# Performance work log

Measured on AMD Instinct MI355X. Metric: run time of the kernel, lower is better.

The kernel has to match this reference:

```python
import jax, jax.numpy as jnp
import numpy as np

N = 100000   # nodes
E = 1000000  # edges
G = 64       # graphs in batch
DIN, DH, DOUT = 128, 128, 64
BN_EPS = 1e-5


def setup_inputs() -> dict:
    key = jax.random.key(0)
    ks = jax.random.split(key, 20)
    inp = {}
    inp['x'] = jax.random.normal(ks[0], (N, DIN), dtype=jnp.float32)
    inp['edge_index'] = jax.random.randint(ks[1], (2, E), 0, N, dtype=jnp.int64)
    inp['batch'] = jnp.sort(jax.random.randint(ks[2], (N,), 0, G, dtype=jnp.int64))
    # GCN conv weights (stored [in, out]) + biases
    s = lambda k, i, o: jax.random.normal(k, (i, o), dtype=jnp.float32) / np.sqrt(i)
    inp['W1'] = s(ks[3], DIN, DH);  inp['b1'] = jnp.zeros((DH,), jnp.float32)
    inp['W2'] = s(ks[4], DH, DH);   inp['b2'] = jnp.zeros((DH,), jnp.float32)
    inp['W3'] = s(ks[5], DH, DOUT); inp['b3'] = jnp.zeros((DOUT,), jnp.float32)
    # BatchNorm params/buffers (eval mode)
    inp['g1'] = jnp.ones((DH,), jnp.float32);  inp['beta1'] = jnp.zeros((DH,), jnp.float32)
    inp['g2'] = jnp.ones((DH,), jnp.float32);  inp['beta2'] = jnp.zeros((DH,), jnp.float32)
    inp['mean1'] = jnp.zeros((DH,), jnp.float32); inp['var1'] = jnp.ones((DH,), jnp.float32)
    inp['mean2'] = jnp.zeros((DH,), jnp.float32); inp['var2'] = jnp.ones((DH,), jnp.float32)
    # GlobalAttention gate_nn: Linear(DOUT,DH) ReLU Linear(DH,1)
    inp['Wg1'] = s(ks[6], DOUT, DH); inp['bg1'] = jnp.zeros((DH,), jnp.float32)
    inp['Wg2'] = s(ks[7], DH, 1);    inp['bg2'] = jnp.zeros((1,), jnp.float32)
    # head MLP: Linear(DOUT,DH) ReLU Linear(DH,DOUT)
    inp['Wm1'] = s(ks[8], DOUT, DH); inp['bm1'] = jnp.zeros((DH,), jnp.float32)
    inp['Wm2'] = s(ks[9], DH, DOUT); inp['bm2'] = jnp.zeros((DOUT,), jnp.float32)
    return inp


def _gcn_conv(x, W, b, src, dst):
    # PyG GCNConv: add self-loops, sym-normalize, linear, scatter-sum, bias
    h = x @ W                                            # [N, out]
    deg = jnp.ones((N,), h.dtype).at[dst].add(1.0)       # in-degree + self-loop
    dinv = jax.lax.rsqrt(deg)
    norm = dinv[src] * dinv[dst]                         # [E]
    msg = h[src] * norm[:, None]                         # gather + scale
    out = jax.ops.segment_sum(msg, dst, num_segments=N)  # scatter
    out = out + h * (dinv * dinv)[:, None]               # self-loop term
    return out + b


def _bn(x, g, beta, mean, var):
    return (x - mean) * jax.lax.rsqrt(var + BN_EPS) * g + beta


def reference(x, edge_index, batch, W1, b1, W2, b2, W3, b3,
              g1, beta1, g2, beta2, mean1, var1, mean2, var2,
              Wg1, bg1, Wg2, bg2, Wm1, bm1, Wm2, bm2):
    src, dst = edge_index[0], edge_index[1]
    h = jax.nn.relu(_bn(_gcn_conv(x, W1, b1, src, dst), g1, beta1, mean1, var1))
    h = jax.nn.relu(_bn(_gcn_conv(h, W2, b2, src, dst), g2, beta2, mean2, var2))
    h = _gcn_conv(h, W3, b3, src, dst)                   # [N, DOUT]
    # GlobalAttention pooling: per-graph softmax of gate scores
    gate = jax.nn.relu(h @ Wg1 + bg1) @ Wg2 + bg2        # [N, 1]
    gate = gate[:, 0]
    m = jax.ops.segment_max(gate, batch, num_segments=G)
    e = jnp.exp(gate - m[batch])
    s = jax.ops.segment_sum(e, batch, num_segments=G)
    a = e / s[batch]                                     # [N]
    pooled = jax.ops.segment_sum(h * a[:, None], batch, num_segments=G)  # [G, DOUT]
    # MLP head (dropout off in eval)
    return jax.nn.relu(pooled @ Wm1 + bm1) @ Wm2 + bm2   # [G, DOUT]
```

## Files before the change

kernel.cpp:

```cpp
#include <hip/hip_runtime.h>
#include <hip/hip_bf16.h>
#include <hip/hip_fp16.h>
#include <math.h>

#define NN 100000
#define EE 1000000
#define GG 64
#define BN_EPS 1e-5f
#define CPB 16
#define EB 4096
#define NBLK ((EE + EB - 1) / EB)
#define NBUCK ((NN + 511) / 512)

typedef __attribute__((ext_vector_type(8))) short bf16x8;
typedef __attribute__((ext_vector_type(4))) float f32x4;

__device__ inline short f2bf(float f) {
  unsigned u = __float_as_uint(f);
  u = u + 0x7fff + ((u >> 16) & 1);
  return (short)(u >> 16);
}
__device__ inline float bf2f(short h) {
  return __uint_as_float(((unsigned)(unsigned short)h) << 16);
}

__device__ inline unsigned fenc(float f) {
  int b = __float_as_int(f);
  return (b < 0) ? ~(unsigned)b : ((unsigned)b | 0x80000000u);
}
__device__ inline float fdec(unsigned u) {
  int b = (u & 0x80000000u) ? (int)(u & 0x7fffffffu) : (int)~u;
  return __int_as_float(b);
}

__device__ inline void acc2(float& a0, float& a1, unsigned u) {
  asm("v_fma_mix_f32 %0, %2, 1.0, %0 op_sel:[0,0,0] op_sel_hi:[1,0,0]\n\t"
      "v_fma_mix_f32 %1, %2, 1.0, %1 op_sel:[1,0,0] op_sel_hi:[1,0,0]"
      : "+v"(a0), "+v"(a1)
      : "v"(u));
}
__device__ inline void acc8(float* a, uint4 u) {
  acc2(a[0], a[1], u.x);
  acc2(a[2], a[3], u.y);
  acc2(a[4], a[5], u.z);
  acc2(a[6], a[7], u.w);
}

__global__ __launch_bounds__(256) void k_bhist(const int* __restrict__ dst,
                                               int* __restrict__ bhist, int E) {
  __shared__ int h[256];
  int t = threadIdx.x;
  h[t] = 0;
  __syncthreads();
  int base = blockIdx.x * EB;
#pragma unroll
  for (int j = 0; j < EB / 256; ++j) {
    int i = base + j * 256 + t;
    if (i < E) atomicAdd(&h[dst[i] >> 9], 1);
  }
  __syncthreads();
  bhist[blockIdx.x * 256 + t] = h[t];
}

__global__ __launch_bounds__(256) void k_bscan1(int* __restrict__ bhist,
                                                int* __restrict__ btot) {
  __shared__ int s[256];
  int bin = blockIdx.x, t = threadIdx.x;
  int v = (t < NBLK) ? bhist[t * 256 + bin] : 0;
  s[t] = v;
  __syncthreads();
  for (int o = 1; o < 256; o <<= 1) {
    int u = (t >= o) ? s[t - o] : 0;
    __syncthreads();
    s[t] += u;
    __syncthreads();
  }
  if (t < NBLK) bhist[t * 256 + bin] = s[t] - v;
  if (t == 255) btot[bin] = s[255];
}

__global__ __launch_bounds__(256) void k_bscan2(const int* __restrict__ btot,
                                                int* __restrict__ bstart) {
  __shared__ int s[256];
  int t = threadIdx.x;
  int v = btot[t];
  s[t] = v;
  __syncthreads();
  for (int o = 1; o < 256; o <<= 1) {
    int u = (t >= o) ? s[t - o] : 0;
    __syncthreads();
    s[t] += u;
    __syncthreads();
  }
  bstart[t] = s[t] - v;
}

__global__ __launch_bounds__(256) void k_bscat(const int* __restrict__ src,
                                               const int* __restrict__ dst,
                                               const int* __restrict__ bhist,
                                               const int* __restrict__ bstart,
                                               int2* __restrict__ pairs, int E) {
  __shared__ int h[256];
  __shared__ int base[256];
  int t = threadIdx.x;
  h[t] = 0;
  __syncthreads();
  int b0 = blockIdx.x * EB;
  int ds[EB / 256], rk[EB / 256];
#pragma unroll
  for (int j = 0; j < EB / 256; ++j) {
    int i = b0 + j * 256 + t;
    if (i < E) {
      int d = dst[i];
      ds[j] = d;
      rk[j] = atomicAdd(&h[d >> 9], 1);
    } else
      ds[j] = -1;
  }
  __syncthreads();
  base[t] = bstart[t] + bhist[blockIdx.x * 256 + t];
  __syncthreads();
#pragma unroll
  for (int j = 0; j < EB / 256; ++j) {
    int i = b0 + j * 256 + t;
    if (ds[j] >= 0) {
      int pos = base[ds[j] >> 9] + rk[j];
      pairs[pos] = make_int2(src[i], ds[j]);
    }
  }
}

__global__ __launch_bounds__(256) void k_bfill(const int2* __restrict__ pairs,
                                               const int* __restrict__ bstart,
                                               int* __restrict__ rowstart,
                                               int* __restrict__ eidx,
                                               float* __restrict__ dinv, int N,
                                               int E) {
  __shared__ int h[512];
  __shared__ int ex[512];
  __shared__ int ps[256];
  const int b = blockIdx.x;
  const int n0 = b << 9;
  const int e0 = bstart[b], e1 = bstart[b + 1];
  const int t = threadIdx.x;
  h[t] = 0;
  h[t + 256] = 0;
  __syncthreads();
  for (int i = e0 + t; i < e1; i += 256) atomicAdd(&h[pairs[i].y - n0], 1);
  __syncthreads();
  int v0 = h[2 * t], v1 = h[2 * t + 1];
  int sp = v0 + v1;
  ps[t] = sp;
  __syncthreads();
  for (int o = 1; o < 256; o <<= 1) {
    int u = (t >= o) ? ps[t - o] : 0;
    __syncthreads();
    ps[t] += u;
    __syncthreads();
  }
  int ex0 = ps[t] - sp;
  ex[2 * t] = ex0;
  ex[2 * t + 1] = ex0 + v0;
  __syncthreads();
  for (int i = t; i < 512; i += 256) {
    int node = n0 + i;
    if (node < N) {
      rowstart[node] = e0 + ex[i];
      dinv[node] = rsqrtf(1.0f + (float)h[i]);
    }
  }
  if (b == 0 && t == 0) rowstart[N] = E;
  __syncthreads();
  for (int i = e0 + t; i < e1; i += 256) {
    int2 p = pairs[i];
    int r = atomicAdd(&ex[p.y - n0], 1);
    eidx[e0 + r] = p.x;
  }
}

__global__ __launch_bounds__(256) void k_wsplit(const float* __restrict__ W1,
                                                const float* __restrict__ W2,
                                                const float* __restrict__ W3,
                                                const float* __restrict__ Wg1,
                                                short* __restrict__ wt) {
  int i = blockIdx.x * 256 + threadIdx.x;
  const float* W;
  short *hi, *lo;
  int K, M, idx;
  if (i < 16384) {
    W = W1; hi = wt; lo = wt + 16384; K = 128; M = 128; idx = i;
  } else if (i < 32768) {
    W = W2; hi = wt + 32768; lo = wt + 49152; K = 128; M = 128; idx = i - 16384;
  } else if (i < 40960) {
    W = W3; hi = wt + 65536; lo = wt + 73728; K = 128; M = 64; idx = i - 32768;
  } else {
    W = Wg1; hi = wt + 81920; lo = wt + 90112; K = 64; M = 128; idx = i - 40960;
  }
  int k = idx / M, n = idx % M;
  float w = W[idx];
  short h = f2bf(w);
  hi[n * K + k] = h;
  lo[n * K + k] = f2bf(w - bf2f(h));
}

__global__ __launch_bounds__(256) void k_bnprep(
    const float* __restrict__ g1, const float* __restrict__ b1,
    const float* __restrict__ m1, const float* __restrict__ v1,
    const float* __restrict__ g2, const float* __restrict__ b2,
    const float* __restrict__ m2, const float* __restrict__ v2,
    float* __restrict__ s1, float* __restrict__ h1, float* __restrict__ s2,
    float* __restrict__ h2) {
  int i = threadIdx.x;
  if (i < 128) {
    float s = g1[i] * rsqrtf(v1[i] + BN_EPS);
    s1[i] = s;
    h1[i] = b1[i] - m1[i] * s;
  } else {
    int j = i - 128;
    float s = g2[j] * rsqrtf(v2[j] + BN_EPS);
    s2[j] = s;
    h2[j] = b2[j] - m2[j] * s;
  }
}

template <int K, int M, int AIN, int DINV, int GATE, int OUTH>
__global__ __launch_bounds__(256, 2) void k_mgemm(
    const float* __restrict__ Xf, const short* __restrict__ Xhi,
    const short* __restrict__ Xlo, const short* __restrict__ Wthi,
    const short* __restrict__ Wtlo, const float* __restrict__ dinv,
    const float* __restrict__ gbias, const float* __restrict__ Wg2v,
    const float* __restrict__ bg2v, void* __restrict__ Y,
    float* __restrict__ gate, int nrows) {
  constexpr int NC = K / 32;
  constexpr int CT = M / 16;
  constexpr int R = 4;
  const int lane = threadIdx.x & 63;
  const int wave = threadIdx.x >> 6;
  const int m16 = lane & 15;
  const int quad = lane >> 4;
  const int rowbase = blockIdx.x * 256 + wave * 64;

  bf16x8 ahi[R][NC], alo[R][NC];
#pragma unroll
  for (int t = 0; t < R; ++t) {
    const int arow = rowbase + t * 16 + m16;
    const bool rok = arow < nrows;
#pragma unroll
    for (int c = 0; c < NC; ++c) {
      const int k0 = c * 32 + quad * 8;
      if constexpr (AIN) {
        if (rok) {
          ahi[t][c] = *(const bf16x8*)(Xhi + (size_t)arow * K + k0);
          alo[t][c] = *(const bf16x8*)(Xlo + (size_t)arow * K + k0);
        } else {
          ahi[t][c] = bf16x8{0, 0, 0, 0, 0, 0, 0, 0};
          alo[t][c] = bf16x8{0, 0, 0, 0, 0, 0, 0, 0};
        }
      } else {
        float4 v0 = make_float4(0.f, 0.f, 0.f, 0.f), v1 = v0;
        if (rok) {
          v0 = *(const float4*)(Xf + (size_t)arow * K + k0);
          v1 = *(const float4*)(Xf + (size_t)arow * K + k0 + 4);
        }
        float vv[8] = {v0.x, v0.y, v0.z, v0.w, v1.x, v1.y, v1.z, v1.w};
#pragma unroll
        for (int j = 0; j < 8; ++j) {
          short h = f2bf(vv[j]);
          ahi[t][c][j] = h;
          alo[t][c][j] = f2bf(vv[j] - bf2f(h));
        }
      }
    }
  }

  float dv[R][4];
  if constexpr (DINV && !GATE) {
#pragma unroll
    for (int t = 0; t < R; ++t)
#pragma unroll
      for (int r = 0; r < 4; ++r) {
        int row = rowbase + t * 16 + quad * 4 + r;
        dv[t][r] = (row < nrows) ? dinv[row] : 0.f;
      }
  }

  float gp[R][4];
  if constexpr (GATE) {
#pragma unroll
    for (int t = 0; t < R; ++t)
#pragma unroll
      for (int r = 0; r < 4; ++r) gp[t][r] = 0.f;
  }

#pragma unroll
  for (int ct = 0; ct < CT; ++ct) {
    bf16x8 bhi[NC], blo[NC];
    const size_t wrow = (size_t)(ct * 16 + m16) * K + quad * 8;
#pragma unroll
    for (int c = 0; c < NC; ++c) {
      bhi[c] = *(const bf16x8*)(Wthi + wrow + c * 32);
      blo[c] = *(const bf16x8*)(Wtlo + wrow + c * 32);
    }
#pragma unroll
    for (int t = 0; t < R; ++t) {
      f32x4 acc = {0.f, 0.f, 0.f, 0.f};
#pragma unroll
      for (int c = 0; c < NC; ++c) {
        acc = __builtin_amdgcn_mfma_f32_16x16x32_bf16(ahi[t][c], bhi[c], acc, 0, 0, 0);
        acc = __builtin_amdgcn_mfma_f32_16x16x32_bf16(ahi[t][c], blo[c], acc, 0, 0, 0);
        acc = __builtin_amdgcn_mfma_f32_16x16x32_bf16(alo[t][c], bhi[c], acc, 0, 0, 0);
      }
      if constexpr (GATE) {
        const int col = ct * 16 + m16;
        const float gb = gbias[col], wg = Wg2v[col];
#pragma unroll
        for (int r = 0; r < 4; ++r) gp[t][r] += fmaxf(acc[r] + gb, 0.f) * wg;
      } else {
#pragma unroll
        for (int r = 0; r < 4; ++r) {
          const int row = rowbase + t * 16 + quad * 4 + r;
          if (row < nrows) {
            float v = acc[r];
            if constexpr (DINV) v *= dv[t][r];
            if constexpr (OUTH)
              ((__half*)Y)[(size_t)row * M + ct * 16 + m16] = __float2half(v);
            else
              ((float*)Y)[(size_t)row * M + ct * 16 + m16] = v;
          }
        }
      }
    }
  }
  if constexpr (GATE) {
#pragma unroll
    for (int o = 1; o < 16; o <<= 1) {
#pragma unroll
      for (int t = 0; t < R; ++t)
#pragma unroll
        for (int r = 0; r < 4; ++r) gp[t][r] += __shfl_xor(gp[t][r], o, 64);
    }
    if (m16 == 0) {
      const float b2 = bg2v[0];
#pragma unroll
      for (int t = 0; t < R; ++t)
#pragma unroll
        for (int r = 0; r < 4; ++r) {
          const int row = rowbase + t * 16 + quad * 4 + r;
          if (row < nrows) gate[row] = gp[t][r] + b2;
        }
    }
  }
}

template <int M, int EPI>
__global__ __launch_bounds__(256) void k_agg(const __half* __restrict__ hp,
                                             const int* __restrict__ rowstart,
                                             const int* __restrict__ eidx,
                                             const float* __restrict__ dinv,
                                             const float* __restrict__ bias,
                                             const float* __restrict__ bns,
                                             const float* __restrict__ bnh,
                                             float* __restrict__ outf,
                                             short* __restrict__ ohi,
                                             short* __restrict__ olo, int N) {
  const int w = (blockIdx.x * 256 + threadIdx.x) >> 6;
  if (w >= N) return;
  const int lane = threadIdx.x & 63;
  constexpr int LPR = M / 8;
  constexpr int EPW = 64 / LPR;
  const int q = lane / LPR;
  const int sub = lane % LPR;
  const unsigned subo = (unsigned)sub * 16u;
  const float di = dinv[w];
  const int lo = rowstart[w], hi = rowstart[w + 1];
  const char* hpb = (const char*)hp;
  float a[8] = {0.f, 0.f, 0.f, 0.f, 0.f, 0.f, 0.f, 0.f};

  int e = lo + q;
  for (; e + EPW < hi; e += 2 * EPW) {
    int s0 = eidx[e], s1 = eidx[e + EPW];
    uint4 u0 = *(const uint4*)(hpb + ((unsigned)s0 * (unsigned)(M * 2) + subo));
    uint4 u1 = *(const uint4*)(hpb + ((unsigned)s1 * (unsigned)(M * 2) + subo));
    acc8(a, u0);
    acc8(a, u1);
  }
  for (; e < hi; e += EPW) {
    int s = eidx[e];
    uint4 u = *(const uint4*)(hpb + ((unsigned)s * (unsigned)(M * 2) + subo));
    acc8(a, u);
  }
#pragma unroll
  for (int o = LPR; o < 64; o <<= 1)
#pragma unroll
    for (int j = 0; j < 8; ++j) a[j] += __shfl_xor(a[j], o, 64);

  if (q != 0) return;
  uint4 us = *(const uint4*)(hpb + ((unsigned)w * (unsigned)(M * 2) + subo));
  acc8(a, us);
  float4 b0 = *(const float4*)(bias + sub * 8);
  float4 b1 = *(const float4*)(bias + sub * 8 + 4);
  float r[8];
  r[0] = a[0] * di + b0.x;
  r[1] = a[1] * di + b0.y;
  r[2] = a[2] * di + b0.z;
  r[3] = a[3] * di + b0.w;
  r[4] = a[4] * di + b1.x;
  r[5] = a[5] * di + b1.y;
  r[6] = a[6] * di + b1.z;
  r[7] = a[7] * di + b1.w;
  if constexpr (EPI) {
    float4 s0 = *(const float4*)(bns + sub * 8);
    float4 s1 = *(const float4*)(bns + sub * 8 + 4);
    float4 h0 = *(const float4*)(bnh + sub * 8);
    float4 h1 = *(const float4*)(bnh + sub * 8 + 4);
    float sv[8] = {s0.x, s0.y, s0.z, s0.w, s1.x, s1.y, s1.z, s1.w};
    float hv[8] = {h0.x, h0.y, h0.z, h0.w, h1.x, h1.y, h1.z, h1.w};
    short hs[8], ls[8];
#pragma unroll
    for (int j = 0; j < 8; ++j) {
      float ev = fmaxf(r[j] * sv[j] + hv[j], 0.f);
      short hb = f2bf(ev);
      float res = ev - bf2f(hb);
      hs[j] = hb;
      ls[j] = (short)(__float_as_uint(res) >> 16);
    }
    *(short4*)(ohi + (size_t)w * M + sub * 8) = make_short4(hs[0], hs[1], hs[2], hs[3]);
    *(short4*)(ohi + (size_t)w * M + sub * 8 + 4) = make_short4(hs[4], hs[5], hs[6], hs[7]);
    *(short4*)(olo + (size_t)w * M + sub * 8) = make_short4(ls[0], ls[1], ls[2], ls[3]);
    *(short4*)(olo + (size_t)w * M + sub * 8 + 4) = make_short4(ls[4], ls[5], ls[6], ls[7]);
  } else {
    *(float4*)(outf + (size_t)w * M + sub * 8) = make_float4(r[0], r[1], r[2], r[3]);
    *(float4*)(outf + (size_t)w * M + sub * 8 + 4) = make_float4(r[4], r[5], r[6], r[7]);
  }
}

__global__ __launch_bounds__(128) void k_gbounds(const int* __restrict__ batch,
                                                 int* __restrict__ gstart,
                                                 int N) {
  int g = threadIdx.x;
  if (g > GG) return;
  int lo = 0, hi = N;
  while (lo < hi) {
    int mid = (lo + hi) >> 1;
    if (batch[mid] < g) lo = mid + 1;
    else hi = mid;
  }
  gstart[g] = lo;
}

__global__ __launch_bounds__(256) void k_pmax(const float* __restrict__ gate,
                                              const int* __restrict__ gstart,
                                              unsigned* __restrict__ gmaxu) {
  __shared__ unsigned red[256];
  const int g = blockIdx.x / CPB;
  const int c = blockIdx.x % CPB;
  const int lo = gstart[g], hi = gstart[g + 1];
  const int len = hi - lo;
  const int b0 = lo + (int)(((long long)len * c) / CPB);
  const int b1 = lo + (int)(((long long)len * (c + 1)) / CPB);
  unsigned mx = 0u;
  for (int i = b0 + threadIdx.x; i < b1; i += 256) mx = max(mx, fenc(gate[i]));
  red[threadIdx.x] = mx;
  __syncthreads();
  for (int o = 128; o; o >>= 1) {
    if (threadIdx.x < o)
      red[threadIdx.x] = max(red[threadIdx.x], red[threadIdx.x + o]);
    __syncthreads();
  }
  if (threadIdx.x == 0 && red[0] != 0u) atomicMax(&gmaxu[g], red[0]);
}

__global__ __launch_bounds__(256) void k_psum(const float* __restrict__ gate,
                                              const float* __restrict__ h3,
                                              const unsigned* __restrict__ gmaxu,
                                              const int* __restrict__ gstart,
                                              float* __restrict__ pooledw,
                                              float* __restrict__ ssum) {
  __shared__ float accs[4][64];
  __shared__ float ses[4];
  const int g = blockIdx.x / CPB;
  const int c = blockIdx.x % CPB;
  const int lo = gstart[g], hi = gstart[g + 1];
  const int len = hi - lo;
  const int b0 = lo + (int)(((long long)len * c) / CPB);
  const int b1 = lo + (int)(((long long)len * (c + 1)) / CPB);
  const int wave = threadIdx.x >> 6, lane = threadIdx.x & 63;
  const float m = fdec(gmaxu[g]);
  float acc = 0.f, se = 0.f;
  for (int i = b0 + wave; i < b1; i += 4) {
    float e = expf(gate[i] - m);
    acc += e * h3[(size_t)i * 64 + lane];
    se += e;
  }
  accs[wave][lane] = acc;
  if (lane == 0) ses[wave] = se;
  __syncthreads();
  if (threadIdx.x < 64) {
    float a = accs[0][threadIdx.x] + accs[1][threadIdx.x] +
              accs[2][threadIdx.x] + accs[3][threadIdx.x];
    if (a != 0.f) atomicAdd(&pooledw[g * 64 + threadIdx.x], a);
  }
  if (threadIdx.x == 64) {
    float s = ses[0] + ses[1] + ses[2] + ses[3];
    if (s != 0.f) atomicAdd(&ssum[g], s);
  }
}

__global__ __launch_bounds__(256) void k_head(const float* __restrict__ pooledw,
                                              const float* __restrict__ ssum,
                                              const float* __restrict__ Wm1,
                                              const float* __restrict__ bm1,
                                              const float* __restrict__ Wm2,
                                              const float* __restrict__ bm2,
                                              float* __restrict__ out) {
  __shared__ float P[64 * 64];
  __shared__ float T[64 * 128];
  int tid = threadIdx.x;
  for (int i = tid; i < 4096; i += 256) {
    float s = ssum[i >> 6];
    P[i] = pooledw[i] * ((s > 0.f) ? 1.0f / s : 0.f);
  }
  __syncthreads();
  for (int e = tid; e < 8192; e += 256) {
    int r = e >> 7, c = e & 127;
    float a = bm1[c];
    for (int k = 0; k < 64; ++k) a += P[r * 64 + k] * Wm1[k * 128 + c];
    T[e] = fmaxf(a, 0.f);
  }
  __syncthreads();
  for (int e = tid; e < 4096; e += 256) {
    int r = e >> 6, c = e & 63;
    float a = bm2[c];
    for (int k = 0; k < 128; ++k) a += T[r * 128 + k] * Wm2[k * 64 + c];
    out[e] = a;
  }
}

extern "C" void kernel_launch(void* const* d_in, const int* in_sizes, int n_in,
                              void* d_out, int out_size, void* d_ws,
                              size_t ws_size, hipStream_t stream) {
  const int N = NN, E = EE;
  const float* x = (const float*)d_in[0];
  const int* ei = (const int*)d_in[1];
  const int* batch = (const int*)d_in[2];
  const float* W1 = (const float*)d_in[3];
  const float* b1 = (const float*)d_in[4];
  const float* W2 = (const float*)d_in[5];
  const float* b2 = (const float*)d_in[6];
  const float* W3 = (const float*)d_in[7];
  const float* b3 = (const float*)d_in[8];
  const float* g1 = (const float*)d_in[9];
  const float* beta1 = (const float*)d_in[10];
  const float* g2 = (const float*)d_in[11];
  const float* beta2 = (const float*)d_in[12];
  const float* mean1 = (const float*)d_in[13];
  const float* var1 = (const float*)d_in[14];
  const float* mean2 = (const float*)d_in[15];
  const float* var2 = (const float*)d_in[16];
  const float* Wg1 = (const float*)d_in[17];
  const float* bg1 = (const float*)d_in[18];
  const float* Wg2 = (const float*)d_in[19];
  const float* bg2 = (const float*)d_in[20];
  const float* Wm1 = (const float*)d_in[21];
  const float* bm1 = (const float*)d_in[22];
  const float* Wm2 = (const float*)d_in[23];
  const float* bm2 = (const float*)d_in[24];
  float* out = (float*)d_out;

  const int* src = ei;
  const int* dst = ei + E;

  char* wsb = (char*)d_ws;
  size_t off = 0;
  auto alloc = [&](size_t elems) -> void* {
    void* p = wsb + off;
    off += elems * 4;
    return p;
  };
  int* rowstart = (int*)alloc(N + 4);
  int* eidx = (int*)alloc(E);
  int2* pairs = (int2*)alloc((size_t)E * 2);
  int* bhist = (int*)alloc(NBLK * 256 + 256);
  int* btot = (int*)alloc(256);
  int* bstart = (int*)alloc(256);
  float* dinv = (float*)alloc(N);
  float* gate = (float*)alloc(N);
  __half* hbuf = (__half*)alloc((size_t)N * 64);
  short* ahi_p = (short*)alloc((size_t)N * 64);
  short* alo_p = (short*)alloc((size_t)N * 64);
  float* fbuf = (float*)alloc((size_t)N * 64);
  short* wt = (short*)alloc(49152);
  float* bn1s = (float*)alloc(128);
  float* bn1h = (float*)alloc(128);
  float* bn2s = (float*)alloc(128);
  float* bn2h = (float*)alloc(128);
  float* pooledw = (float*)alloc(GG * 64);
  float* ssum = (float*)alloc(GG);
  unsigned* gmaxu = (unsigned*)alloc(GG);
  int* gstart = (int*)alloc(GG + 4);
  (void)ws_size;
  (void)n_in;
  (void)in_sizes;
  (void)out_size;

  hipMemsetAsync(pooledw, 0, (GG * 64 + GG + GG) * sizeof(float), stream);
  k_bhist<<<NBLK, 256, 0, stream>>>(dst, bhist, E);
  k_bscan1<<<256, 256, 0, stream>>>(bhist, btot);
  k_bscan2<<<1, 256, 0, stream>>>(btot, bstart);
  k_bscat<<<NBLK, 256, 0, stream>>>(src, dst, bhist, bstart, pairs, E);
  k_bfill<<<NBUCK, 256, 0, stream>>>(pairs, bstart, rowstart, eidx, dinv, N, E);

  k_wsplit<<<192, 256, 0, stream>>>(W1, W2, W3, Wg1, wt);
  k_bnprep<<<1, 256, 0, stream>>>(g1, beta1, mean1, var1, g2, beta2, mean2,
                                  var2, bn1s, bn1h, bn2s, bn2h);
  k_gbounds<<<1, 128, 0, stream>>>(batch, gstart, N);

  const int gb = (N + 255) / 256;
  const int ab = (N * 64 + 255) / 256;

  k_mgemm<128, 128, 0, 1, 0, 1><<<gb, 256, 0, stream>>>(
      x, nullptr, nullptr, wt, wt + 16384, dinv, nullptr, nullptr, nullptr,
      hbuf, nullptr, N);
  k_agg<128, 1><<<ab, 256, 0, stream>>>(hbuf, rowstart, eidx, dinv, b1, bn1s,
                                        bn1h, nullptr, ahi_p, alo_p, N);

  k_mgemm<128, 128, 1, 1, 0, 1><<<gb, 256, 0, stream>>>(
      nullptr, ahi_p, alo_p, wt + 32768, wt + 49152, dinv, nullptr, nullptr,
      nullptr, hbuf, nullptr, N);
  k_agg<128, 1><<<ab, 256, 0, stream>>>(hbuf, rowstart, eidx, dinv, b2, bn2s,
                                        bn2h, nullptr, ahi_p, alo_p, N);

  k_mgemm<128, 64, 1, 1, 0, 1><<<gb, 256, 0, stream>>>(
      nullptr, ahi_p, alo_p, wt + 65536, wt + 73728, dinv, nullptr, nullptr,
      nullptr, hbuf, nullptr, N);
  k_agg<64, 0><<<ab, 256, 0, stream>>>(hbuf, rowstart, eidx, dinv, b3, nullptr,
                                       nullptr, fbuf, nullptr, nullptr, N);

  k_mgemm<64, 128, 0, 0, 1, 0><<<gb, 256, 0, stream>>>(
      fbuf, nullptr, nullptr, wt + 81920, wt + 90112, nullptr, bg1, Wg2, bg2,
      nullptr, gate, N);

  k_pmax<<<GG * CPB, 256, 0, stream>>>(gate, gstart, gmaxu);
  k_psum<<<GG * CPB, 256, 0, stream>>>(gate, fbuf, gmaxu, gstart, pooledw,
                                       ssum);

  k_head<<<1, 256, 0, stream>>>(pooledw, ssum, Wm1, bm1, Wm2, bm2, out);
}
```

Measured before the change: 497.4 us.

## Pack multiple nodes per wavefront in GCN aggregation with unrolled masked gathers

```diff
diff --git a/kernel.cpp b/kernel.cpp
--- a/kernel.cpp
+++ b/kernel.cpp
@@ -44,6 +44,14 @@
   acc2(a[2], a[3], u.y);
   acc2(a[4], a[5], u.z);
   acc2(a[6], a[7], u.w);
+}
+__device__ inline uint4 zsel(uint4 u, int ok) {
+  uint4 r;
+  r.x = ok ? u.x : 0u;
+  r.y = ok ? u.y : 0u;
+  r.z = ok ? u.z : 0u;
+  r.w = ok ? u.w : 0u;
+  return r;
 }
 
 __global__ __launch_bounds__(256) void k_bhist(const int* __restrict__ dst,
@@ -363,38 +371,47 @@
                                              float* __restrict__ outf,
                                              short* __restrict__ ohi,
                                              short* __restrict__ olo, int N) {
-  const int w = (blockIdx.x * 256 + threadIdx.x) >> 6;
+  constexpr int LPR = M / 8;
+  constexpr int NPW = 64 / (2 * LPR);
+  const int wv = (blockIdx.x * 256 + threadIdx.x) >> 6;
+  const int lane = threadIdx.x & 63;
+  const int grp = lane / (2 * LPR);
+  const int slot = (lane / LPR) & 1;
+  const int sub = lane % LPR;
+  const int w = wv * NPW + grp;
   if (w >= N) return;
-  const int lane = threadIdx.x & 63;
-  constexpr int LPR = M / 8;
-  constexpr int EPW = 64 / LPR;
-  const int q = lane / LPR;
-  const int sub = lane % LPR;
   const unsigned subo = (unsigned)sub * 16u;
   const float di = dinv[w];
   const int lo = rowstart[w], hi = rowstart[w + 1];
+  const int hi1 = hi - 1;
   const char* hpb = (const char*)hp;
   float a[8] = {0.f, 0.f, 0.f, 0.f, 0.f, 0.f, 0.f, 0.f};
 
-  int e = lo + q;
-  for (; e + EPW < hi; e += 2 * EPW) {
-    int s0 = eidx[e], s1 = eidx[e + EPW];
+  int e = lo + slot;
+  while (e < hi) {
+    int i0 = e, i1 = e + 2, i2 = e + 4, i3 = e + 6;
+    int s0 = eidx[min(i0, hi1)];
+    int s1 = eidx[min(i1, hi1)];
+    int s2 = eidx[min(i2, hi1)];
+    int s3 = eidx[min(i3, hi1)];
     uint4 u0 = *(const uint4*)(hpb + ((unsigned)s0 * (unsigned)(M * 2) + subo));
     uint4 u1 = *(const uint4*)(hpb + ((unsigned)s1 * (unsigned)(M * 2) + subo));
+    uint4 u2 = *(const uint4*)(hpb + ((unsigned)s2 * (unsigned)(M * 2) + subo));
+    uint4 u3 = *(const uint4*)(hpb + ((unsigned)s3 * (unsigned)(M * 2) + subo));
+    u0 = zsel(u0, i0 < hi);
+    u1 = zsel(u1, i1 < hi);
+    u2 = zsel(u2, i2 < hi);
+    u3 = zsel(u3, i3 < hi);
     acc8(a, u0);
     acc8(a, u1);
-  }
-  for (; e < hi; e += EPW) {
-    int s = eidx[e];
-    uint4 u = *(const uint4*)(hpb + ((unsigned)s * (unsigned)(M * 2) + subo));
-    acc8(a, u);
-  }
-#pragma unroll
-  for (int o = LPR; o < 64; o <<= 1)
-#pragma unroll
-    for (int j = 0; j < 8; ++j) a[j] += __shfl_xor(a[j], o, 64);
-
-  if (q != 0) return;
+    acc8(a, u2);
+    acc8(a, u3);
+    e += 8;
+  }
+#pragma unroll
+  for (int j = 0; j < 8; ++j) a[j] += __shfl_xor(a[j], LPR, 64);
+
+  if (slot != 0) return;
   uint4 us = *(const uint4*)(hpb + ((unsigned)w * (unsigned)(M * 2) + subo));
   acc8(a, us);
   float4 b0 = *(const float4*)(bias + sub * 8);
@@ -616,25 +633,29 @@
   k_gbounds<<<1, 128, 0, stream>>>(batch, gstart, N);
 
   const int gb = (N + 255) / 256;
-  const int ab = (N * 64 + 255) / 256;
+  const int ab128 = (N + 7) / 8;
+  const int ab64 = (N + 15) / 16;
 
   k_mgemm<128, 128, 0, 1, 0, 1><<<gb, 256, 0, stream>>>(
       x, nullptr, nullptr, wt, wt + 16384, dinv, nullptr, nullptr, nullptr,
       hbuf, nullptr, N);
-  k_agg<128, 1><<<ab, 256, 0, stream>>>(hbuf, rowstart, eidx, dinv, b1, bn1s,
-                                        bn1h, nullptr, ahi_p, alo_p, N);
+  k_agg<128, 1><<<ab128, 256, 0, stream>>>(hbuf, rowstart, eidx, dinv, b1,
+                                           bn1s, bn1h, nullptr, ahi_p, alo_p,
+                                           N);
 
   k_mgemm<128, 128, 1, 1, 0, 1><<<gb, 256, 0, stream>>>(
       nullptr, ahi_p, alo_p, wt + 32768, wt + 49152, dinv, nullptr, nullptr,
       nullptr, hbuf, nullptr, N);
-  k_agg<128, 1><<<ab, 256, 0, stream>>>(hbuf, rowstart, eidx, dinv, b2, bn2s,
-                                        bn2h, nullptr, ahi_p, alo_p, N);
+  k_agg<128, 1><<<ab128, 256, 0, stream>>>(hbuf, rowstart, eidx, dinv, b2,
+                                           bn2s, bn2h, nullptr, ahi_p, alo_p,
+                                           N);
 
   k_mgemm<128, 64, 1, 1, 0, 1><<<gb, 256, 0, stream>>>(
       nullptr, ahi_p, alo_p, wt + 65536, wt + 73728, dinv, nullptr, nullptr,
       nullptr, hbuf, nullptr, N);
-  k_agg<64, 0><<<ab, 256, 0, stream>>>(hbuf, rowstart, eidx, dinv, b3, nullptr,
-                                       nullptr, fbuf, nullptr, nullptr, N);
+  k_agg<64, 0><<<ab64, 256, 0, stream>>>(hbuf, rowstart, eidx, dinv, b3,
+                                         nullptr, nullptr, fbuf, nullptr,
+                                         nullptr, N);
 
   k_mgemm<64, 128, 0, 0, 1, 0><<<gb, 256, 0, stream>>>(
       fbuf, nullptr, nullptr, wt + 81920, wt + 90112, nullptr, bg1, Wg2, bg2,
```

Result: faster. 478.7 us (-3.8%).
